# Optimization experiments

Measured on AMD Instinct MI355X. Metric: run time of the kernel, lower is better.

Reference implementation:

```python
import jax, jax.numpy as jnp
import numpy as np

N = 50000    # total nodes in a batched graph
E = 200000   # directed edges (before self loops)
G = 256      # molecules per batch
F_IN = 64    # atom features
H = 4        # gat heads
CH = 128     # hidden_channels (per head)
D = H * CH   # 512, concat width
MLP_H = 128  # hidden_channels * mlp_hidden_factor
NEG_SLOPE = 0.2


def _gat(x, src, dst, W, a_src, a_dst, b, concat):
    """PyG GATConv (eval mode, self loops already added to src/dst)."""
    n = x.shape[0]
    heads, ch = a_src.shape
    h = (x @ W).reshape(n, heads, ch)                       # [N,H,C]
    e = jax.nn.leaky_relu((h * a_src).sum(-1)[src]
                          + (h * a_dst).sum(-1)[dst], NEG_SLOPE)  # [E,H]
    emax = jax.ops.segment_max(e, dst, num_segments=n)
    emax = jnp.where(jnp.isfinite(emax), emax, 0.0)
    p = jnp.exp(e - emax[dst])
    denom = jax.ops.segment_sum(p, dst, num_segments=n)
    alpha = p / (denom[dst] + 1e-16)                        # segment softmax over dst
    out = jax.ops.segment_sum(h[src] * alpha[..., None], dst, num_segments=n)
    out = out.reshape(n, heads * ch) if concat else out.mean(axis=1)
    return out + b


def _encoder(x, edge_index, batch, p):
    n = x.shape[0]
    loop = jnp.arange(n, dtype=edge_index.dtype)            # GATConv add_self_loops=True
    src = jnp.concatenate([edge_index[0], loop])
    dst = jnp.concatenate([edge_index[1], loop])
    x = jax.nn.elu(_gat(x, src, dst, p['W1'], p['as1'], p['ad1'], p['b1'], True))
    x = jax.nn.elu(_gat(x, src, dst, p['W2'], p['as2'], p['ad2'], p['b2'], True))
    x = _gat(x, src, dst, p['W3'], p['as3'], p['ad3'], p['b3'], False)
    emb = jax.ops.segment_max(x, batch, num_segments=G)     # global_max_pool
    return jnp.where(jnp.isfinite(emb), emb, 0.0)


def setup_inputs() -> dict:
    key = jax.random.key(0)
    ks = jax.random.split(key, 24)
    rn = lambda k, s, sc=0.1: jax.random.normal(k, s, jnp.float32) * sc
    return dict(
        x1=rn(ks[0], (N, F_IN), 1.0),
        edge_index1=jax.random.randint(ks[1], (2, E), 0, N, dtype=jnp.int32),
        batch1=jnp.sort(jax.random.randint(ks[2], (N,), 0, G, dtype=jnp.int32)),
        x2=rn(ks[3], (N, F_IN), 1.0),
        edge_index2=jax.random.randint(ks[4], (2, E), 0, N, dtype=jnp.int32),
        batch2=jnp.sort(jax.random.randint(ks[5], (N,), 0, G, dtype=jnp.int32)),
        W1=rn(ks[6], (F_IN, D)), as1=rn(ks[7], (H, CH)), ad1=rn(ks[8], (H, CH)),
        b1=jnp.zeros((D,), jnp.float32),
        W2=rn(ks[9], (D, D)), as2=rn(ks[10], (H, CH)), ad2=rn(ks[11], (H, CH)),
        b2=jnp.zeros((D,), jnp.float32),
        W3=rn(ks[12], (D, CH)), as3=rn(ks[13], (1, CH)), ad3=rn(ks[14], (1, CH)),
        b3=jnp.zeros((CH,), jnp.float32),
        mw1=rn(ks[15], (2 * CH, MLP_H)), mb1=jnp.zeros((MLP_H,), jnp.float32),
        mw2=rn(ks[16], (MLP_H, 1)), mb2=jnp.zeros((1,), jnp.float32),
    )


def reference(x1, edge_index1, batch1, x2, edge_index2, batch2,
              W1, as1, ad1, b1, W2, as2, ad2, b2, W3, as3, ad3, b3,
              mw1, mb1, mw2, mb2):
    p = dict(W1=W1, as1=as1, ad1=ad1, b1=b1,
             W2=W2, as2=as2, ad2=ad2, b2=b2,
             W3=W3, as3=as3, ad3=ad3, b3=b3)
    e1 = _encoder(x1, edge_index1, batch1, p)               # [G, CH]
    e2 = _encoder(x2, edge_index2, batch2, p)               # [G, CH]
    z = jnp.concatenate([e1, e2], axis=-1)                  # [G, 2*CH]
    return jax.nn.relu(z @ mw1 + mb1) @ mw2 + mb2           # [G, 1]
```

## Files before the change

kernel.cpp:

```cpp
#include <hip/hip_runtime.h>
#include <cstdint>

namespace {
constexpr int kN = 50000;
constexpr int kE = 200000;
constexpr int kE2 = kE + kN;
constexpr int kG = 256;
constexpr float kNegSlope = 0.2f;
}

using half8   = __attribute__((ext_vector_type(8))) _Float16;
using floatx4 = __attribute__((ext_vector_type(4))) float;

__device__ __forceinline__ void gld_lds16(const void* g, void* l) {
  __builtin_amdgcn_global_load_lds(
      (const __attribute__((address_space(1))) unsigned int*)g,
      (__attribute__((address_space(3))) unsigned int*)l, 16, 0, 0);
}

__device__ __forceinline__ float fexp(float x) {
  return __builtin_amdgcn_exp2f(x * 1.44269504088896f);
}

template <int OUTF16, int NT>
__global__ __launch_bounds__(256, 4) void gemm_f16(
    const _Float16* __restrict__ A, const _Float16* __restrict__ B,
    void* __restrict__ Cv, int M, int N, int K) {
  __shared__ alignas(16) char smem[32768];
  const int t = threadIdx.x;
  const int w = t >> 6;
  const int l = t & 63;
  int bm, bn;
  if constexpr (NT == 1) {
    bm = blockIdx.x * 128;
    bn = 0;
  } else {
    const int x = blockIdx.x & 7;
    const int s = blockIdx.x >> 3;
    bm = (((s >> 2) << 3) + x) * 128;
    bn = (s & 3) * 128;
    if (bm >= M) return;
  }
  const int wm = (w & 1) * 64;
  const int wn = (w >> 1) * 64;
  const int quad = l >> 4;
  const int lrow = l & 15;

  floatx4 acc[4][4];
#pragma unroll
  for (int mi = 0; mi < 4; ++mi)
#pragma unroll
    for (int ni = 0; ni < 4; ++ni) acc[mi][ni] = (floatx4){0.f, 0.f, 0.f, 0.f};

  auto stage = [&](char* sbuf, int k0) {
#pragma unroll
    for (int j = 0; j < 2; ++j) {
      const int s = w * 128 + j * 64 + l;
      const int row = ((s >> 6) << 4) + (s & 15);
      const int q = (s >> 4) & 3;
      int ga = bm + row;
      ga = (ga < M) ? ga : (M - 1);
      gld_lds16(A + (size_t)ga * K + k0 + q * 8, sbuf + s * 16);
      gld_lds16(B + (size_t)(bn + row) * K + k0 + q * 8, sbuf + 8192 + s * 16);
    }
  };

  stage(smem, 0);
  int cur = 0;
  for (int k0 = 0; k0 < K; k0 += 32) {
    char* sA = smem + cur * 16384;
    char* sB = sA + 8192;
    if (k0 + 32 < K) {
      stage(smem + ((cur ^ 1) * 16384), k0 + 32);
      asm volatile("s_waitcnt vmcnt(4)" ::: "memory");
    } else {
      asm volatile("s_waitcnt vmcnt(0)" ::: "memory");
    }
    __builtin_amdgcn_s_barrier();
    asm volatile("" ::: "memory");
    half8 fa[4], fb[4];
#pragma unroll
    for (int mi = 0; mi < 4; ++mi)
      fa[mi] = *(const half8*)(sA + ((wm >> 4) + mi) * 1024 + l * 16);
#pragma unroll
    for (int ni = 0; ni < 4; ++ni)
      fb[ni] = *(const half8*)(sB + ((wn >> 4) + ni) * 1024 + l * 16);
#pragma unroll
    for (int mi = 0; mi < 4; ++mi)
#pragma unroll
      for (int ni = 0; ni < 4; ++ni)
        acc[mi][ni] = __builtin_amdgcn_mfma_f32_16x16x32_f16(fa[mi], fb[ni],
                                                             acc[mi][ni], 0, 0, 0);
    asm volatile("" ::: "memory");
    __builtin_amdgcn_s_barrier();
    cur ^= 1;
  }
  const int colbase = bn + wn + lrow;
#pragma unroll
  for (int mi = 0; mi < 4; ++mi) {
    const int rbase = bm + wm + mi * 16 + quad * 4;
#pragma unroll
    for (int r = 0; r < 4; ++r) {
      const int grow = rbase + r;
      if (grow < M) {
        if constexpr (OUTF16) {
          _Float16* C = (_Float16*)Cv;
#pragma unroll
          for (int ni = 0; ni < 4; ++ni)
            C[(size_t)grow * N + colbase + ni * 16] = (_Float16)acc[mi][ni][r];
        } else {
          float* C = (float*)Cv;
#pragma unroll
          for (int ni = 0; ni < 4; ++ni)
            C[(size_t)grow * N + colbase + ni * 16] = acc[mi][ni][r];
        }
      }
    }
  }
}

__global__ void wt_split_all(const float* __restrict__ W1, _Float16* Th1,
                             const float* __restrict__ W2, _Float16* Th2,
                             const float* __restrict__ W3, _Float16* Th3) {
  int idx = blockIdx.x * blockDim.x + threadIdx.x;
  const float* W;
  _Float16* Th;
  int K, N;
  if (idx < 64 * 512) {
    W = W1; Th = Th1; K = 64; N = 512;
  } else if (idx < 64 * 512 + 512 * 512) {
    idx -= 64 * 512;
    W = W2; Th = Th2; K = 512; N = 512;
  } else if (idx < 64 * 512 + 512 * 512 + 512 * 128) {
    idx -= 64 * 512 + 512 * 512;
    W = W3; Th = Th3; K = 512; N = 128;
  } else {
    return;
  }
  const int k = idx / N;
  const int n = idx - k * N;
  Th[n * K + k] = (_Float16)W[idx];
}

__global__ void prep2(const float* __restrict__ x0, const float* __restrict__ x1,
                      _Float16* __restrict__ Xh, int* __restrict__ cnt,
                      int* __restrict__ total) {
  const int idx = blockIdx.x * blockDim.x + threadIdx.x;
  const int half = kN * 64;
  if (idx < half) Xh[idx] = (_Float16)x0[idx];
  else if (idx < 2 * half) Xh[idx] = (_Float16)x1[idx - half];
  if (idx < 2 * kN) cnt[idx] = 1;
  if (idx == 0) *total = 0;
}
__global__ void prep(const float* __restrict__ X, _Float16* __restrict__ Xh,
                     int* __restrict__ cnt, int* __restrict__ total, int nsplit,
                     int n) {
  const int idx = blockIdx.x * blockDim.x + threadIdx.x;
  if (idx < nsplit) Xh[idx] = (_Float16)X[idx];
  if (idx < n) cnt[idx] = 1;
  if (idx == 0) *total = 0;
}

__global__ void count_edges2(const int* __restrict__ d0, const int* __restrict__ d1,
                             int* __restrict__ cnt) {
  const int i = blockIdx.x * blockDim.x + threadIdx.x;
  if (i < kE) atomicAdd(&cnt[d0[i]], 1);
  else if (i < 2 * kE) atomicAdd(&cnt[d1[i - kE] + kN], 1);
}
__global__ void fill_edges2(const int* __restrict__ s0, const int* __restrict__ d0,
                            const int* __restrict__ s1, const int* __restrict__ d1,
                            int* __restrict__ cursor, int* __restrict__ csr) {
  const int i = blockIdx.x * blockDim.x + threadIdx.x;
  if (i < kE) {
    const int p = atomicAdd(&cursor[d0[i]], 1);
    csr[p] = s0[i];
  } else if (i < 2 * kE) {
    const int j = i - kE;
    const int p = atomicAdd(&cursor[d1[j] + kN], 1);
    csr[p] = s1[j] + kN;
  }
}
__global__ void count_edges(const int* __restrict__ dst, int* __restrict__ cnt,
                            int ne) {
  const int i = blockIdx.x * blockDim.x + threadIdx.x;
  if (i < ne) atomicAdd(&cnt[dst[i]], 1);
}
__global__ void fill_edges(const int* __restrict__ src, const int* __restrict__ dst,
                           int* __restrict__ cursor, int* __restrict__ csr, int ne) {
  const int i = blockIdx.x * blockDim.x + threadIdx.x;
  if (i < ne) {
    const int p = atomicAdd(&cursor[dst[i]], 1);
    csr[p] = src[i];
  }
}
__global__ void alloc_ranges(const int* __restrict__ cnt, int* __restrict__ start,
                             int* __restrict__ cursor, int* __restrict__ total,
                             int* __restrict__ csr, int n) {
  const int i = blockIdx.x * blockDim.x + threadIdx.x;
  const int lane = threadIdx.x & 63;
  const int v = (i < n) ? cnt[i] : 0;
  int sc = v;
#pragma unroll
  for (int off = 1; off < 64; off <<= 1) {
    const int t = __shfl_up(sc, off);
    if (lane >= off) sc += t;
  }
  const int wtot = __shfl(sc, 63);
  int base = 0;
  if (lane == 63) base = atomicAdd(total, wtot);
  base = __shfl(base, 63);
  const int st = base + sc - v;
  if (i < n) {
    start[i] = st;
    cursor[i] = st + 1;
    csr[st] = i;
  }
}

__global__ void gat_agg4(const _Float16* __restrict__ h,
                         const float* __restrict__ a_src,
                         const float* __restrict__ a_dst,
                         const int* __restrict__ start, const int* __restrict__ cnt,
                         const int* __restrict__ csr_src,
                         const float* __restrict__ bias,
                         _Float16* __restrict__ outH, int n_nodes) {
  const int gtid = blockIdx.x * blockDim.x + threadIdx.x;
  const int node = gtid >> 6;
  const int lane = threadIdx.x & 63;
  if (node >= n_nodes) return;
  const int ch = lane * 8;
  float as_r[8], ad_r[8];
#pragma unroll
  for (int j = 0; j < 8; ++j) {
    as_r[j] = a_src[ch + j];
    ad_r[j] = a_dst[ch + j];
  }
  const int s = start[node];
  const int c = cnt[node];
  const half8 vs = *(const half8*)(h + (size_t)node * 512 + ch);
  float fs[8];
  float t_src = 0.f, t_dst = 0.f;
#pragma unroll
  for (int j = 0; j < 8; ++j) {
    fs[j] = (float)vs[j];
    t_src = fmaf(fs[j], as_r[j], t_src);
    t_dst = fmaf(fs[j], ad_r[j], t_dst);
  }
#pragma unroll
  for (int off = 1; off < 16; off <<= 1) {
    t_src += __shfl_xor(t_src, off);
    t_dst += __shfl_xor(t_dst, off);
  }
  const float ad = t_dst;
  float es = t_src + ad;
  es = (es > 0.f) ? es : kNegSlope * es;
  const float ws = fexp(es);
  float d0 = ws, d1 = 0.f;
  float a0[8], a1[8];
#pragma unroll
  for (int j = 0; j < 8; ++j) {
    a0[j] = ws * fs[j];
    a1[j] = 0.f;
  }
  int i = 1;
  for (; i + 2 <= c; i += 2) {
    const int s0 = csr_src[s + i];
    const int s1 = csr_src[s + i + 1];
    const half8 v0 = *(const half8*)(h + (size_t)s0 * 512 + ch);
    const half8 v1 = *(const half8*)(h + (size_t)s1 * 512 + ch);
    float f0[8], f1[8];
    float t0 = 0.f, t1 = 0.f;
#pragma unroll
    for (int j = 0; j < 8; ++j) {
      f0[j] = (float)v0[j];
      f1[j] = (float)v1[j];
      t0 = fmaf(f0[j], as_r[j], t0);
      t1 = fmaf(f1[j], as_r[j], t1);
    }
#pragma unroll
    for (int off = 1; off < 16; off <<= 1) {
      t0 += __shfl_xor(t0, off);
      t1 += __shfl_xor(t1, off);
    }
    float e0 = t0 + ad;
    float e1 = t1 + ad;
    e0 = (e0 > 0.f) ? e0 : kNegSlope * e0;
    e1 = (e1 > 0.f) ? e1 : kNegSlope * e1;
    const float w0 = fexp(e0);
    const float w1 = fexp(e1);
    d0 += w0;
    d1 += w1;
#pragma unroll
    for (int j = 0; j < 8; ++j) {
      a0[j] = fmaf(w0, f0[j], a0[j]);
      a1[j] = fmaf(w1, f1[j], a1[j]);
    }
  }
  if (i < c) {
    const int s0 = csr_src[s + i];
    const half8 v0 = *(const half8*)(h + (size_t)s0 * 512 + ch);
    float f0[8];
    float t0 = 0.f;
#pragma unroll
    for (int j = 0; j < 8; ++j) {
      f0[j] = (float)v0[j];
      t0 = fmaf(f0[j], as_r[j], t0);
    }
#pragma unroll
    for (int off = 1; off < 16; off <<= 1) t0 += __shfl_xor(t0, off);
    float e0 = t0 + ad;
    e0 = (e0 > 0.f) ? e0 : kNegSlope * e0;
    const float w0 = fexp(e0);
    d0 += w0;
#pragma unroll
    for (int j = 0; j < 8; ++j) a0[j] = fmaf(w0, f0[j], a0[j]);
  }
  const float inv = 1.f / (d0 + d1 + 1e-16f);
  half8 H;
#pragma unroll
  for (int j = 0; j < 8; ++j) {
    float v = (a0[j] + a1[j]) * inv + bias[ch + j];
    v = (v > 0.f) ? v : (fexp(v) - 1.f);
    H[j] = (_Float16)v;
  }
  *(half8*)(outH + (size_t)node * 512 + ch) = H;
}

__global__ void gat_agg_l3(const float* __restrict__ h,
                           const float* __restrict__ a_src,
                           const float* __restrict__ a_dst,
                           const int* __restrict__ start, const int* __restrict__ cnt,
                           const int* __restrict__ csr_src,
                           const float* __restrict__ bias,
                           float* __restrict__ out, int n_nodes) {
  const int gtid = blockIdx.x * blockDim.x + threadIdx.x;
  const int node = gtid >> 6;
  const int lane = threadIdx.x & 63;
  if (node >= n_nodes) return;
  const float2 asv = *(const float2*)(a_src + lane * 2);
  const float2 adv = *(const float2*)(a_dst + lane * 2);
  const int s = start[node];
  const int c = cnt[node];
  const float2 vs = *(const float2*)(h + (size_t)node * 128 + lane * 2);
  float t_src = fmaf(vs.x, asv.x, vs.y * asv.y);
  float t_dst = fmaf(vs.x, adv.x, vs.y * adv.y);
#pragma unroll
  for (int off = 1; off < 64; off <<= 1) {
    t_src += __shfl_xor(t_src, off);
    t_dst += __shfl_xor(t_dst, off);
  }
  const float ad = t_dst;
  float es = t_src + ad;
  es = (es > 0.f) ? es : kNegSlope * es;
  const float ws = fexp(es);
  float2 a0 = make_float2(ws * vs.x, ws * vs.y);
  float2 a1 = make_float2(0.f, 0.f);
  float d0 = ws, d1 = 0.f;
  int i = 1;
  for (; i + 2 <= c; i += 2) {
    const int s0 = csr_src[s + i];
    const int s1 = csr_src[s + i + 1];
    const float2 v0 = *(const float2*)(h + (size_t)s0 * 128 + lane * 2);
    const float2 v1 = *(const float2*)(h + (size_t)s1 * 128 + lane * 2);
    float t0 = fmaf(v0.x, asv.x, v0.y * asv.y);
    float t1 = fmaf(v1.x, asv.x, v1.y * asv.y);
#pragma unroll
    for (int off = 1; off < 64; off <<= 1) {
      t0 += __shfl_xor(t0, off);
      t1 += __shfl_xor(t1, off);
    }
    float e0 = t0 + ad;
    float e1 = t1 + ad;
    e0 = (e0 > 0.f) ? e0 : kNegSlope * e0;
    e1 = (e1 > 0.f) ? e1 : kNegSlope * e1;
    const float w0 = fexp(e0);
    const float w1 = fexp(e1);
    d0 += w0;
    d1 += w1;
    a0.x = fmaf(w0, v0.x, a0.x); a1.x = fmaf(w1, v1.x, a1.x);
    a0.y = fmaf(w0, v0.y, a0.y); a1.y = fmaf(w1, v1.y, a1.y);
  }
  if (i < c) {
    const int s0 = csr_src[s + i];
    const float2 v0 = *(const float2*)(h + (size_t)s0 * 128 + lane * 2);
    float t0 = fmaf(v0.x, asv.x, v0.y * asv.y);
#pragma unroll
    for (int off = 1; off < 64; off <<= 1) t0 += __shfl_xor(t0, off);
    float e0 = t0 + ad;
    e0 = (e0 > 0.f) ? e0 : kNegSlope * e0;
    const float w0 = fexp(e0);
    d0 += w0;
    a0.x = fmaf(w0, v0.x, a0.x);
    a0.y = fmaf(w0, v0.y, a0.y);
  }
  const float inv = 1.f / (d0 + d1 + 1e-16f);
  *(float2*)(out + (size_t)node * 128 + lane * 2) =
      make_float2((a0.x + a1.x) * inv + bias[lane * 2],
                  (a0.y + a1.y) * inv + bias[lane * 2 + 1]);
}

__global__ void pool_max(const float* __restrict__ x, const int* __restrict__ batch,
                         float* __restrict__ emb, int n_nodes) {
  __shared__ int lohi[2];
  const int g = blockIdx.x;
  if (threadIdx.x == 0) {
    int lo = 0, hi = n_nodes;
    while (lo < hi) {
      const int mid = (lo + hi) >> 1;
      if (batch[mid] < g) lo = mid + 1; else hi = mid;
    }
    lohi[0] = lo;
    hi = n_nodes;
    while (lo < hi) {
      const int mid = (lo + hi) >> 1;
      if (batch[mid] < g + 1) lo = mid + 1; else hi = mid;
    }
    lohi[1] = lo;
  }
  __syncthreads();
  const int lo = lohi[0], hi = lohi[1];
  const int c = threadIdx.x;
  float m = -1e30f;
  for (int nid = lo; nid < hi; ++nid) m = fmaxf(m, x[(size_t)nid * 128 + c]);
  emb[g * 128 + c] = (lo < hi) ? m : 0.f;
}

__global__ void mlp_head(const float* __restrict__ e1, const float* __restrict__ e2,
                         const float* __restrict__ mw1, const float* __restrict__ mb1,
                         const float* __restrict__ mw2, const float* __restrict__ mb2,
                         float* __restrict__ out) {
  __shared__ float z[256];
  __shared__ float red[128];
  const int g = blockIdx.x;
  const int j = threadIdx.x;
  z[j] = e1[g * 128 + j];
  z[j + 128] = e2[g * 128 + j];
  __syncthreads();
  float acc = mb1[j];
  for (int k = 0; k < 256; ++k) acc = fmaf(z[k], mw1[k * 128 + j], acc);
  acc = fmaxf(acc, 0.f) * mw2[j];
  red[j] = acc;
  __syncthreads();
  for (int s = 64; s > 0; s >>= 1) {
    if (j < s) red[j] += red[j + s];
    __syncthreads();
  }
  if (j == 0) out[g] = red[0] + mb2[0];
}

namespace {
struct Bufs {
  _Float16 *R1h, *R2h;
  float *R1f, *R2f, *asrc, *adst;
  int *cnt, *start, *cursor, *csr, *total;
  _Float16 *Wth1, *Wth2, *Wth3;
  float* emb;
  size_t need;
};

Bufs plan(void* d_ws, int M, int E) {
  Bufs b;
  char* w = (char*)d_ws;
  size_t off = 0;
  auto take = [&](size_t bytes) -> void* {
    void* p = w + off;
    off += (bytes + 255) & ~(size_t)255;
    return p;
  };
  b.R1h = (_Float16*)take((size_t)M * 512 * 2);
  b.R1f = (float*)b.R1h;
  b.R2h = (_Float16*)take((size_t)M * 512 * 2);
  b.R2f = (float*)b.R2h;
  b.asrc = (float*)take((size_t)M * 4 * 4);
  b.adst = (float*)take((size_t)M * 4 * 4);
  b.cnt = (int*)take((size_t)M * 4);
  b.start = (int*)take((size_t)M * 4);
  b.cursor = (int*)take((size_t)M * 4);
  b.csr = (int*)take((size_t)E * 4);
  b.total = (int*)take(256);
  b.Wth1 = (_Float16*)take((size_t)64 * 512 * 2);
  b.Wth2 = (_Float16*)take((size_t)512 * 512 * 2);
  b.Wth3 = (_Float16*)take((size_t)512 * 128 * 2);
  b.emb = (float*)take((size_t)2 * kG * 128 * 4);
  b.need = off;
  return b;
}

void run_layers(const Bufs& b, void* const* d_in, int M, hipStream_t stream) {
  const float* as1 = (const float*)d_in[7];
  const float* ad1 = (const float*)d_in[8];
  const float* b1 = (const float*)d_in[9];
  const float* as2 = (const float*)d_in[11];
  const float* ad2 = (const float*)d_in[12];
  const float* b2 = (const float*)d_in[13];
  const float* as3 = (const float*)d_in[15];
  const float* ad3 = (const float*)d_in[16];
  const float* b3 = (const float*)d_in[17];
  const int nodeBlocks = (M * 64) / 256;
  const int MT = (M + 127) / 128;
  const int MTp = (MT + 7) & ~7;

  gemm_f16<1, 4><<<MTp * 4, 256, 0, stream>>>(b.R1h, b.Wth1, b.R2h, M, 512, 64);
  gat_agg4<<<nodeBlocks, 256, 0, stream>>>(b.R2h, as1, ad1, b.start, b.cnt,
                                           b.csr, b1, b.R1h, M);
  gemm_f16<1, 4><<<MTp * 4, 256, 0, stream>>>(b.R1h, b.Wth2, b.R2h, M, 512, 512);
  gat_agg4<<<nodeBlocks, 256, 0, stream>>>(b.R2h, as2, ad2, b.start, b.cnt,
                                           b.csr, b2, b.R1h, M);
  gemm_f16<0, 1><<<MT, 256, 0, stream>>>(b.R1h, b.Wth3, b.R2f, M, 128, 512);
  gat_agg_l3<<<nodeBlocks, 256, 0, stream>>>(b.R2f, as3, ad3, b.start, b.cnt,
                                             b.csr, b3, b.R1f, M);
}
}

extern "C" void kernel_launch(void* const* d_in, const int* in_sizes, int n_in,
                              void* d_out, int out_size, void* d_ws, size_t ws_size,
                              hipStream_t stream) {
  (void)in_sizes; (void)n_in; (void)out_size;
  const float* W1 = (const float*)d_in[6];
  const float* W2 = (const float*)d_in[10];
  const float* W3 = (const float*)d_in[14];
  const float* mw1 = (const float*)d_in[18];
  const float* mb1 = (const float*)d_in[19];
  const float* mw2 = (const float*)d_in[20];
  const float* mb2 = (const float*)d_in[21];

  Bufs bc = plan(d_ws, 2 * kN, 2 * kE2);
  const bool combined = bc.need <= ws_size;
  Bufs b = combined ? bc : plan(d_ws, kN, kE2);

  const int wtot = 64 * 512 + 512 * 512 + 512 * 128;
  wt_split_all<<<(wtot + 255) / 256, 256, 0, stream>>>(W1, b.Wth1, W2, b.Wth2, W3,
                                                       b.Wth3);
  if (combined) {
    const int M = 2 * kN;
    const int* ei0 = (const int*)d_in[1];
    const int* ei1 = (const int*)d_in[4];
    prep2<<<(2 * kN * 64 + 255) / 256, 256, 0, stream>>>(
        (const float*)d_in[0], (const float*)d_in[3], b.R1h, b.cnt, b.total);
    count_edges2<<<(2 * kE + 255) / 256, 256, 0, stream>>>(ei0 + kE, ei1 + kE,
                                                           b.cnt);
    alloc_ranges<<<(M + 255) / 256, 256, 0, stream>>>(b.cnt, b.start, b.cursor,
                                                      b.total, b.csr, M);
    fill_edges2<<<(2 * kE + 255) / 256, 256, 0, stream>>>(ei0, ei0 + kE, ei1,
                                                          ei1 + kE, b.cursor, b.csr);
    run_layers(b, d_in, M, stream);
    for (int enc = 0; enc < 2; ++enc) {
      const int* batch = (const int*)d_in[enc * 3 + 2];
      pool_max<<<kG, 128, 0, stream>>>(b.R1f + (size_t)enc * kN * 128, batch,
                                       b.emb + (size_t)enc * kG * 128, kN);
    }
  } else {
    for (int enc = 0; enc < 2; ++enc) {
      const float* x = (const float*)d_in[enc * 3 + 0];
      const int* ei = (const int*)d_in[enc * 3 + 1];
      const int* batch = (const int*)d_in[enc * 3 + 2];
      prep<<<(kN * 64 + 255) / 256, 256, 0, stream>>>(x, b.R1h, b.cnt, b.total,
                                                      kN * 64, kN);
      count_edges<<<(kE + 255) / 256, 256, 0, stream>>>(ei + kE, b.cnt, kE);
      alloc_ranges<<<(kN + 255) / 256, 256, 0, stream>>>(b.cnt, b.start, b.cursor,
                                                         b.total, b.csr, kN);
      fill_edges<<<(kE + 255) / 256, 256, 0, stream>>>(ei, ei + kE, b.cursor, b.csr,
                                                       kE);
      run_layers(b, d_in, kN, stream);
      pool_max<<<kG, 128, 0, stream>>>(b.R1f, batch, b.emb + (size_t)enc * kG * 128,
                                       kN);
    }
  }
  mlp_head<<<kG, 128, 0, stream>>>(b.emb, b.emb + (size_t)kG * 128, mw1, mb1, mw2,
                                   mb2, (float*)d_out);
}
```

Baseline: 703.9 us.

## Enlarge GEMM tiles to 256 rows with 512 threads and K=64 stages

```diff
diff --git a/kernel.cpp b/kernel.cpp
--- a/kernel.cpp
+++ b/kernel.cpp
@@ -22,83 +22,104 @@
   return __builtin_amdgcn_exp2f(x * 1.44269504088896f);
 }
 
-template <int OUTF16, int NT>
-__global__ __launch_bounds__(256, 4) void gemm_f16(
+template <int OUTF16, int BN, int CT>
+__global__ __launch_bounds__(512, 2) void gemm256(
     const _Float16* __restrict__ A, const _Float16* __restrict__ B,
     void* __restrict__ Cv, int M, int N, int K) {
-  __shared__ alignas(16) char smem[32768];
+  constexpr int ASLOTS = 2048;
+  constexpr int BSLOTS = BN * 8;
+  constexpr int LPT = (ASLOTS + BSLOTS) / 512;
+  constexpr int BUFB = (ASLOTS + BSLOTS) * 16;
+  constexpr int WN = (BN == 256) ? 4 : 2;
+  constexpr int WM = 8 / WN;
+  constexpr int WTM = 256 / WM;
+  constexpr int WTN = BN / WN;
+  constexpr int MI = WTM / 16;
+  constexpr int NI = WTN / 16;
+  __shared__ alignas(16) char smem[2 * BUFB];
   const int t = threadIdx.x;
-  const int w = t >> 6;
-  const int l = t & 63;
-  int bm, bn;
-  if constexpr (NT == 1) {
-    bm = blockIdx.x * 128;
-    bn = 0;
-  } else {
-    const int x = blockIdx.x & 7;
-    const int s = blockIdx.x >> 3;
-    bm = (((s >> 2) << 3) + x) * 128;
-    bn = (s & 3) * 128;
-    if (bm >= M) return;
-  }
-  const int wm = (w & 1) * 64;
-  const int wn = (w >> 1) * 64;
-  const int quad = l >> 4;
-  const int lrow = l & 15;
-
-  floatx4 acc[4][4];
-#pragma unroll
-  for (int mi = 0; mi < 4; ++mi)
-#pragma unroll
-    for (int ni = 0; ni < 4; ++ni) acc[mi][ni] = (floatx4){0.f, 0.f, 0.f, 0.f};
-
-  auto stage = [&](char* sbuf, int k0) {
-#pragma unroll
-    for (int j = 0; j < 2; ++j) {
-      const int s = w * 128 + j * 64 + l;
-      const int row = ((s >> 6) << 4) + (s & 15);
-      const int q = (s >> 4) & 3;
+  const int w = t >> 6, l = t & 63;
+  const int x = blockIdx.x & 7, s = blockIdx.x >> 3;
+  const int col = (CT == 1) ? 0 : (s & (CT - 1));
+  const int rt = ((CT == 1) ? s : (s >> 1)) * 8 + x;
+  const int bm = rt * 256;
+  const int bn = col * BN;
+  if (bm >= M) return;
+  const int wr = w / WN, wc = w % WN;
+  const int quad = l >> 4, lrow = l & 15;
+
+  floatx4 acc[MI][NI];
+#pragma unroll
+  for (int mi = 0; mi < MI; ++mi)
+#pragma unroll
+    for (int ni = 0; ni < NI; ++ni) acc[mi][ni] = (floatx4){0.f, 0.f, 0.f, 0.f};
+
+  auto stage = [&](char* buf, int k0) {
+#pragma unroll
+    for (int i = 0; i < ASLOTS / 512; ++i) {
+      const int sl = i * 512 + t;
+      const int kh = sl >> 10;
+      const int r = sl & 1023;
+      const int row = ((r >> 6) << 4) + (r & 15);
+      const int q = (r >> 4) & 3;
       int ga = bm + row;
       ga = (ga < M) ? ga : (M - 1);
-      gld_lds16(A + (size_t)ga * K + k0 + q * 8, sbuf + s * 16);
-      gld_lds16(B + (size_t)(bn + row) * K + k0 + q * 8, sbuf + 8192 + s * 16);
+      gld_lds16(A + (size_t)ga * K + k0 + kh * 32 + q * 8, buf + sl * 16);
+    }
+#pragma unroll
+    for (int i = 0; i < BSLOTS / 512; ++i) {
+      const int sl = i * 512 + t;
+      const int kh = sl / (BSLOTS / 2);
+      const int r = sl % (BSLOTS / 2);
+      const int row = ((r >> 6) << 4) + (r & 15);
+      const int q = (r >> 4) & 3;
+      gld_lds16(B + (size_t)(bn + row) * K + k0 + kh * 32 + q * 8,
+                buf + (ASLOTS + sl) * 16);
     }
   };
 
   stage(smem, 0);
   int cur = 0;
-  for (int k0 = 0; k0 < K; k0 += 32) {
-    char* sA = smem + cur * 16384;
-    char* sB = sA + 8192;
-    if (k0 + 32 < K) {
-      stage(smem + ((cur ^ 1) * 16384), k0 + 32);
-      asm volatile("s_waitcnt vmcnt(4)" ::: "memory");
+  for (int k0 = 0; k0 < K; k0 += 64) {
+    char* bufc = smem + cur * BUFB;
+    if (k0 + 64 < K) {
+      stage(smem + (cur ^ 1) * BUFB, k0 + 64);
+      if constexpr (LPT == 8)
+        asm volatile("s_waitcnt vmcnt(8)" ::: "memory");
+      else
+        asm volatile("s_waitcnt vmcnt(6)" ::: "memory");
     } else {
       asm volatile("s_waitcnt vmcnt(0)" ::: "memory");
     }
     __builtin_amdgcn_s_barrier();
     asm volatile("" ::: "memory");
-    half8 fa[4], fb[4];
-#pragma unroll
-    for (int mi = 0; mi < 4; ++mi)
-      fa[mi] = *(const half8*)(sA + ((wm >> 4) + mi) * 1024 + l * 16);
-#pragma unroll
-    for (int ni = 0; ni < 4; ++ni)
-      fb[ni] = *(const half8*)(sB + ((wn >> 4) + ni) * 1024 + l * 16);
-#pragma unroll
-    for (int mi = 0; mi < 4; ++mi)
-#pragma unroll
-      for (int ni = 0; ni < 4; ++ni)
-        acc[mi][ni] = __builtin_amdgcn_mfma_f32_16x16x32_f16(fa[mi], fb[ni],
-                                                             acc[mi][ni], 0, 0, 0);
+#pragma unroll
+    for (int kh = 0; kh < 2; ++kh) {
+      half8 fa[MI], fb[NI];
+#pragma unroll
+      for (int mi = 0; mi < MI; ++mi)
+        fa[mi] = *(const half8*)(bufc + ((kh * 16 + wr * MI + mi) << 10) + l * 16);
+#pragma unroll
+      for (int ni = 0; ni < NI; ++ni)
+        fb[ni] = *(const half8*)(bufc + ASLOTS * 16 +
+                                 ((kh * (BN / 16) + wc * NI + ni) << 10) + l * 16);
+      __builtin_amdgcn_s_setprio(1);
+#pragma unroll
+      for (int mi = 0; mi < MI; ++mi)
+#pragma unroll
+        for (int ni = 0; ni < NI; ++ni)
+          acc[mi][ni] = __builtin_amdgcn_mfma_f32_16x16x32_f16(
+              fa[mi], fb[ni], acc[mi][ni], 0, 0, 0);
+      __builtin_amdgcn_s_setprio(0);
+    }
     asm volatile("" ::: "memory");
     __builtin_amdgcn_s_barrier();
     cur ^= 1;
   }
-  const int colbase = bn + wn + lrow;
-#pragma unroll
-  for (int mi = 0; mi < 4; ++mi) {
-    const int rbase = bm + wm + mi * 16 + quad * 4;
+  const int colbase = bn + wc * WTN + lrow;
+#pragma unroll
+  for (int mi = 0; mi < MI; ++mi) {
+    const int rbase = bm + wr * WTM + mi * 16 + quad * 4;
 #pragma unroll
     for (int r = 0; r < 4; ++r) {
       const int grow = rbase + r;
@@ -106,12 +127,12 @@
         if constexpr (OUTF16) {
           _Float16* C = (_Float16*)Cv;
 #pragma unroll
-          for (int ni = 0; ni < 4; ++ni)
+          for (int ni = 0; ni < NI; ++ni)
             C[(size_t)grow * N + colbase + ni * 16] = (_Float16)acc[mi][ni][r];
         } else {
           float* C = (float*)Cv;
 #pragma unroll
-          for (int ni = 0; ni < 4; ++ni)
+          for (int ni = 0; ni < NI; ++ni)
             C[(size_t)grow * N + colbase + ni * 16] = acc[mi][ni][r];
         }
       }
@@ -497,16 +518,16 @@
   const float* ad3 = (const float*)d_in[16];
   const float* b3 = (const float*)d_in[17];
   const int nodeBlocks = (M * 64) / 256;
-  const int MT = (M + 127) / 128;
-  const int MTp = (MT + 7) & ~7;
-
-  gemm_f16<1, 4><<<MTp * 4, 256, 0, stream>>>(b.R1h, b.Wth1, b.R2h, M, 512, 64);
+  const int MT = (M + 255) / 256;
+  const int SP = (MT + 7) / 8;
+
+  gemm256<1, 256, 2><<<SP * 16, 512, 0, stream>>>(b.R1h, b.Wth1, b.R2h, M, 512, 64);
   gat_agg4<<<nodeBlocks, 256, 0, stream>>>(b.R2h, as1, ad1, b.start, b.cnt,
                                            b.csr, b1, b.R1h, M);
-  gemm_f16<1, 4><<<MTp * 4, 256, 0, stream>>>(b.R1h, b.Wth2, b.R2h, M, 512, 512);
+  gemm256<1, 256, 2><<<SP * 16, 512, 0, stream>>>(b.R1h, b.Wth2, b.R2h, M, 512, 512);
   gat_agg4<<<nodeBlocks, 256, 0, stream>>>(b.R2h, as2, ad2, b.start, b.cnt,
                                            b.csr, b2, b.R1h, M);
-  gemm_f16<0, 1><<<MT, 256, 0, stream>>>(b.R1h, b.Wth3, b.R2f, M, 128, 512);
+  gemm256<0, 128, 1><<<SP * 8, 512, 0, stream>>>(b.R1h, b.Wth3, b.R2f, M, 128, 512);
   gat_agg_l3<<<nodeBlocks, 256, 0, stream>>>(b.R2f, as3, ad3, b.start, b.cnt,
                                              b.csr, b3, b.R1f, M);
 }
```

Result: no change. 695.5 us (-1.2%).
